# Kernel optimization log

Hardware: AMD Instinct MI355X
Metric: run time of the kernel (lower is better)

Reference implementation:

```python
import jax, jax.numpy as jnp
import numpy as np

H = 16          # num_heads
W = 256         # attention_window
D_MODEL = 1024
D_FF = 4096
EPS = 1e-5


def _layernorm(x, g, b):
    mu = jnp.mean(x, axis=-1, keepdims=True)
    var = jnp.mean(jnp.square(x - mu), axis=-1, keepdims=True)
    return (x - mu) * jax.lax.rsqrt(var + EPS) * g + b


def _sliding_attn(q, k, v, w):
    # q,k,v: [B,H,S,d]; each query attends to keys in [i-w, i+w]
    B, Hh, S, d = q.shape
    nc = S // w
    qc = q.reshape(B, Hh, nc, w, d)
    kp = jnp.pad(k, ((0, 0), (0, 0), (w, w), (0, 0)))
    vp = jnp.pad(v, ((0, 0), (0, 0), (w, w), (0, 0)))
    # gather 3w keys per chunk (prev w, current w, next w)
    idx = (jnp.arange(nc) * w)[:, None] + jnp.arange(3 * w)[None, :]  # [nc, 3w]
    kc = kp[:, :, idx, :]  # [B,H,nc,3w,d]
    vc = vp[:, :, idx, :]
    scores = jnp.einsum('bhcqd,bhckd->bhcqk', qc, kc)  # [B,H,nc,w,3w]
    q_pos = jnp.arange(nc)[:, None, None] * w + jnp.arange(w)[None, :, None]
    k_pos = jnp.arange(nc)[:, None, None] * w - w + jnp.arange(3 * w)[None, None, :]
    rel = k_pos - q_pos
    valid = (jnp.abs(rel) <= w) & (k_pos >= 0) & (k_pos < S)  # [nc,w,3w]
    scores = jnp.where(valid[None, None], scores, jnp.float32(-1e9))
    p = jax.nn.softmax(scores, axis=-1)
    out = jnp.einsum('bhcqk,bhckd->bhcqd', p, vc)
    return out.reshape(B, Hh, S, d)


def setup_inputs() -> dict:
    key = jax.random.key(0)
    ks = jax.random.split(key, 8)
    B, S = 2, 4096
    src = jax.random.normal(ks[0], (B, S, D_MODEL), dtype=jnp.float32)
    ln1_g = jnp.ones((D_MODEL,), jnp.float32)
    ln1_b = jnp.zeros((D_MODEL,), jnp.float32)
    ln2_g = jnp.ones((D_MODEL,), jnp.float32)
    ln2_b = jnp.zeros((D_MODEL,), jnp.float32)
    W1 = jax.random.normal(ks[1], (D_MODEL, D_FF), jnp.float32) * 0.02
    b1 = jnp.zeros((D_FF,), jnp.float32)
    W2 = jax.random.normal(ks[2], (D_FF, D_MODEL), jnp.float32) * 0.02
    b2 = jnp.zeros((D_MODEL,), jnp.float32)
    return {"src": src, "ln1_g": ln1_g, "ln1_b": ln1_b, "ln2_g": ln2_g,
            "ln2_b": ln2_b, "W1": W1, "b1": b1, "W2": W2, "b2": b2}


def reference(src, ln1_g, ln1_b, ln2_g, ln2_b, W1, b1, W2, b2):
    B, S, _ = src.shape
    d_head = D_MODEL // H
    qkv = src.reshape(B, S, H, d_head).transpose(0, 2, 1, 3)  # [B,H,S,d]
    attn = _sliding_attn(qkv, qkv, qkv, W)
    attn = attn.transpose(0, 2, 1, 3).reshape(B, S, D_MODEL)
    x = _layernorm(src + attn, ln1_g, ln1_b)
    ff = jnp.maximum(x @ W1 + b1, 0.0) @ W2 + b2
    return _layernorm(x + ff, ln2_g, ln2_b)
```

## Files before the change

kernel.cpp:

```cpp
#include <hip/hip_runtime.h>

typedef __bf16 bf16x8 __attribute__((ext_vector_type(8)));
typedef __bf16 bf16x4 __attribute__((ext_vector_type(4)));
typedef float f32x4 __attribute__((ext_vector_type(4)));

#define MFMA16(a, b, c) __builtin_amdgcn_mfma_f32_16x16x32_bf16((a), (b), (c), 0, 0, 0)

__device__ __forceinline__ void gload_lds16(const void* g, void* l) {
  __builtin_amdgcn_global_load_lds(
      (const __attribute__((address_space(1))) unsigned int*)g,
      (__attribute__((address_space(3))) unsigned int*)l, 16, 0, 0);
}

__global__ __launch_bounds__(512, 2) void attn_kernel(const float* __restrict__ src,
                                                      float* __restrict__ attn_out) {
  const int bid = blockIdx.x;
  const int c = bid & 15;
  const int h = (bid >> 4) & 15;
  const int b = bid >> 8;
  const int tid = threadIdx.x;
  const int w = tid >> 6;
  const int lane = tid & 63;
  const int lg = lane >> 4;
  const int l16 = lane & 15;
  const size_t b4096 = (size_t)b * 4096;

  __shared__ __bf16 Ks[64][72];
  __shared__ __bf16 Vt[64][72];

  const int q0 = c * 256 + w * 32;
  const float LOG2E = 1.44269504f;

  bf16x8 qf[2][2];
#pragma unroll
  for (int qfi = 0; qfi < 2; ++qfi)
#pragma unroll
    for (int ks = 0; ks < 2; ++ks) {
      const int row = q0 + qfi * 16 + l16;
      const int d0 = ks * 32 + lg * 8;
      const float* p = src + (b4096 + row) * 1024 + h * 64 + d0;
      bf16x8 v;
#pragma unroll
      for (int j = 0; j < 8; ++j) v[j] = (__bf16)(p[j] * LOG2E);
      qf[qfi][ks] = v;
    }

  int krow[4];
#pragma unroll
  for (int kf = 0; kf < 4; ++kf)
    krow[kf] = ((kf >> 1) << 5) + ((l16 >> 2) << 3) + ((kf & 1) << 2) + (l16 & 3);

  const f32x4 z4 = {0.f, 0.f, 0.f, 0.f};
  float m_run[2], l_run[2];
  f32x4 o[2][4];
#pragma unroll
  for (int qfi = 0; qfi < 2; ++qfi) {
    m_run[qfi] = -6.0e8f;
    l_run[qfi] = 0.f;
#pragma unroll
    for (int df = 0; df < 4; ++df) o[qfi][df] = z4;
  }

  const int stage_key = tid >> 3;
  const int stage_d0 = (tid & 7) * 8;
  const int vcol = stage_key ^ stage_d0;

  int kpos = c * 256 - 256 + stage_key;
  float4 ga, gb;
  {
    const int rc = min(max(kpos, 0), 4095);
    const float* p = src + (b4096 + rc) * 1024 + h * 64 + stage_d0;
    ga = *(const float4*)p;
    gb = *(const float4*)(p + 4);
  }

  for (int kt = 0; kt < 12; ++kt) {
    const int kbase = c * 256 - 256 + kt * 64;
    bf16x8 kv;
    const bool inb = ((unsigned)kpos < 4096u);
    kv[0] = (__bf16)(inb ? ga.x : 0.f); kv[1] = (__bf16)(inb ? ga.y : 0.f);
    kv[2] = (__bf16)(inb ? ga.z : 0.f); kv[3] = (__bf16)(inb ? ga.w : 0.f);
    kv[4] = (__bf16)(inb ? gb.x : 0.f); kv[5] = (__bf16)(inb ? gb.y : 0.f);
    kv[6] = (__bf16)(inb ? gb.z : 0.f); kv[7] = (__bf16)(inb ? gb.w : 0.f);

    __syncthreads();
    *(bf16x8*)&Ks[stage_key][stage_d0] = kv;
#pragma unroll
    for (int j = 0; j < 8; ++j) Vt[stage_d0 + j][vcol] = kv[j];
    asm volatile("s_waitcnt lgkmcnt(0)" ::: "memory");
    __builtin_amdgcn_s_barrier();
    __builtin_amdgcn_sched_barrier(0);

    kpos += 64;
    if (kt < 11) {
      const int rc = min(max(kpos, 0), 4095);
      const float* p = src + (b4096 + rc) * 1024 + h * 64 + stage_d0;
      ga = *(const float4*)p;
      gb = *(const float4*)(p + 4);
    }

    const bool skip = (kbase + 63 < 0) | (kbase >= 4096) |
                      (kbase + 63 < q0 - 256) | (kbase > q0 + 31 + 256);
    if (skip) continue;

    f32x4 s[4][2];
#pragma unroll
    for (int kf = 0; kf < 4; ++kf)
#pragma unroll
      for (int qfi = 0; qfi < 2; ++qfi) s[kf][qfi] = z4;

#pragma unroll
    for (int ks = 0; ks < 2; ++ks) {
      bf16x8 ka[4];
#pragma unroll
      for (int kf = 0; kf < 4; ++kf)
        ka[kf] = *(const bf16x8*)&Ks[krow[kf]][ks * 32 + lg * 8];
#pragma unroll
      for (int kf = 0; kf < 4; ++kf)
#pragma unroll
        for (int qfi = 0; qfi < 2; ++qfi)
          s[kf][qfi] = MFMA16(ka[kf], qf[qfi][ks], s[kf][qfi]);
    }

    const bool needmask = (kbase < 0) | (kbase > 4032) |
                          (kbase < q0 - 225) | (kbase > q0 + 193);
    if (needmask) {
#pragma unroll
      for (int qfi = 0; qfi < 2; ++qfi) {
        const int qp = q0 + qfi * 16 + l16;
#pragma unroll
        for (int kf = 0; kf < 4; ++kf) {
          const int kb0 = kbase + ((kf >> 1) << 5) + 8 * lg + ((kf & 1) << 2);
#pragma unroll
          for (int reg = 0; reg < 4; ++reg) {
            const int kp = kb0 + reg;
            const int rel = kp - qp;
            if (rel > 256 || rel < -256 || kp < 0 || kp >= 4096)
              s[kf][qfi][reg] = -1e9f;
          }
        }
      }
    }

    bf16x4 pb[4][2];
#pragma unroll
    for (int qfi = 0; qfi < 2; ++qfi) {
      float tm = s[0][qfi][0];
#pragma unroll
      for (int kf = 0; kf < 4; ++kf)
#pragma unroll
        for (int reg = 0; reg < 4; ++reg) tm = fmaxf(tm, s[kf][qfi][reg]);
      tm = fmaxf(tm, __shfl_xor(tm, 16, 64));
      tm = fmaxf(tm, __shfl_xor(tm, 32, 64));

      const float mn = fmaxf(m_run[qfi], tm);
      const float scl = exp2f(m_run[qfi] - mn);
      m_run[qfi] = mn;

      float rs = 0.f;
#pragma unroll
      for (int kf = 0; kf < 4; ++kf) {
        bf16x4 pv;
#pragma unroll
        for (int reg = 0; reg < 4; ++reg) {
          const float p = exp2f(s[kf][qfi][reg] - mn);
          rs += p;
          pv[reg] = (__bf16)p;
        }
        pb[kf][qfi] = pv;
      }
      rs += __shfl_xor(rs, 16, 64);
      rs += __shfl_xor(rs, 32, 64);
      l_run[qfi] = l_run[qfi] * scl + rs;

#pragma unroll
      for (int df = 0; df < 4; ++df)
#pragma unroll
        for (int reg = 0; reg < 4; ++reg) o[qfi][df][reg] *= scl;
    }

#pragma unroll
    for (int ks2 = 0; ks2 < 2; ++ks2) {
      bf16x8 av[4];
#pragma unroll
      for (int df = 0; df < 4; ++df) {
        const int d = df * 16 + l16;
        const int blk = (ks2 * 4 + lg) ^ (d >> 3);
        av[df] = *(const bf16x8*)&Vt[d][blk * 8];
      }
#pragma unroll
      for (int qfi = 0; qfi < 2; ++qfi) {
        const bf16x8 bq = __builtin_shufflevector(pb[2 * ks2][qfi], pb[2 * ks2 + 1][qfi],
                                                  0, 1, 2, 3, 4, 5, 6, 7);
#pragma unroll
        for (int df = 0; df < 4; ++df)
          o[qfi][df] = MFMA16(av[df], bq, o[qfi][df]);
      }
    }
  }

#pragma unroll
  for (int qfi = 0; qfi < 2; ++qfi) {
    const float inv = 1.0f / l_run[qfi];
    const int qp = q0 + qfi * 16 + l16;
    float* dst = attn_out + (b4096 + qp) * 1024 + h * 64 + lg * 4;
#pragma unroll
    for (int df = 0; df < 4; ++df) {
      float4 r;
      r.x = o[qfi][df][0] * inv;
      r.y = o[qfi][df][1] * inv;
      r.z = o[qfi][df][2] * inv;
      r.w = o[qfi][df][3] * inv;
      *(float4*)&dst[df * 16] = r;
    }
  }
}

template <int MODE>
__global__ __launch_bounds__(512, 2) void gemm8p(const __bf16* __restrict__ A,
                                                 const __bf16* __restrict__ Bt,
                                                 const float* __restrict__ bias,
                                                 void* __restrict__ out0,
                                                 void* __restrict__ out1,
                                                 int M, int N, int Kstride, int Klen) {
  __shared__ char smem[131072];
  const int tid = threadIdx.x;
  const int w = tid >> 6;
  const int lane = tid & 63;
  const int lg = lane >> 4;
  const int l16 = lane & 15;
  const int wr = w >> 2;
  const int wc = w & 3;

  const int nbn = N >> 8;
  const int x = ((int)blockIdx.x & 7) * ((int)gridDim.x >> 3) + ((int)blockIdx.x >> 3);
  const long bm = (long)(x / nbn) * 256;
  const long bn = (long)(x % nbn) * 256;
  const long koff = (long)blockIdx.y * Klen;
  void* out = blockIdx.y ? out1 : out0;

  const f32x4 z4 = {0.f, 0.f, 0.f, 0.f};
  f32x4 acc[8][4];
#pragma unroll
  for (int i = 0; i < 8; ++i)
#pragma unroll
    for (int j = 0; j < 4; ++j) acc[i][j] = z4;

  const int srow = tid >> 2;
  const int g0 = (tid & 3) ^ ((tid >> 3) & 3);
  const __bf16* Ag = A + (size_t)(bm + srow) * Kstride + koff + g0 * 8;
  const __bf16* Bg = Bt + (size_t)(bn + srow) * Kstride + koff + g0 * 8;

  auto stage = [&](int kt, int osel, int isB, int khalf) {
    const __bf16* src = (isB ? Bg : Ag) + (size_t)kt * 64 + khalf * 32;
    char* dst = smem + (isB ? 65536 : 0) + osel * 32768 + khalf * 16384 + (w << 10);
    gload_lds16(src, dst);
    gload_lds16(src + (size_t)128 * Kstride, dst + 8192);
  };

  const int lslot = (lg ^ ((l16 >> 1) & 3)) << 4;
  const char* pA = smem + (wr * 128 + l16) * 64 + lslot;
  const char* pB = smem + 65536 + (wc * 64 + l16) * 64 + lslot;
  auto rdA = [&](int sel, int rf, int ks) {
    return *(const bf16x8*)(pA + sel * 32768 + ks * 16384 + rf * 1024);
  };
  auto rdB = [&](int sel, int cf, int ks) {
    return *(const bf16x8*)(pB + sel * 32768 + ks * 16384 + cf * 1024);
  };

  const int NT = Klen >> 6;

  stage(0, 0, 0, 0);
  stage(0, 0, 1, 0);
  stage(0, 0, 0, 1);
  stage(0, 0, 1, 1);
  asm volatile("s_waitcnt vmcnt(4)" ::: "memory");
  __builtin_amdgcn_s_barrier();
  __builtin_amdgcn_sched_barrier(0);

  for (int t = 0; t < NT; ++t) {
    const int sel = t & 1, osel = sel ^ 1;
    const bool st = (t + 1) < NT;
    bf16x8 af[8], bf[4];

#pragma unroll
    for (int rf = 0; rf < 8; ++rf) af[rf] = rdA(sel, rf, 0);
#pragma unroll
    for (int cf = 0; cf < 4; ++cf) bf[cf] = rdB(sel, cf, 0);
    if (st) { stage(t + 1, osel, 0, 0); stage(t + 1, osel, 1, 0); }
    __builtin_amdgcn_s_setprio(1);
#pragma unroll
    for (int rf = 0; rf < 8; ++rf)
#pragma unroll
      for (int cf = 0; cf < 4; ++cf)
        acc[rf][cf] = MFMA16(af[rf], bf[cf], acc[rf][cf]);
    __builtin_amdgcn_s_setprio(0);
    if (st) asm volatile("s_waitcnt vmcnt(4)" ::: "memory");
    else    asm volatile("s_waitcnt vmcnt(0)" ::: "memory");
    __builtin_amdgcn_s_barrier();
    __builtin_amdgcn_sched_barrier(0);

#pragma unroll
    for (int rf = 0; rf < 8; ++rf) af[rf] = rdA(sel, rf, 1);
#pragma unroll
    for (int cf = 0; cf < 4; ++cf) bf[cf] = rdB(sel, cf, 1);
    if (st) { stage(t + 1, osel, 0, 1); stage(t + 1, osel, 1, 1); }
    __builtin_amdgcn_s_setprio(1);
#pragma unroll
    for (int rf = 0; rf < 8; ++rf)
#pragma unroll
      for (int cf = 0; cf < 4; ++cf)
        acc[rf][cf] = MFMA16(af[rf], bf[cf], acc[rf][cf]);
    __builtin_amdgcn_s_setprio(0);
    if (st) asm volatile("s_waitcnt vmcnt(4)" ::: "memory");
    __builtin_amdgcn_s_barrier();
    __builtin_amdgcn_sched_barrier(0);
  }

  float bv[4];
  if (MODE == 0) {
#pragma unroll
    for (int cf = 0; cf < 4; ++cf) bv[cf] = bias[bn + wc * 64 + cf * 16 + l16];
  }
#pragma unroll
  for (int rf = 0; rf < 8; ++rf)
#pragma unroll
    for (int reg = 0; reg < 4; ++reg) {
      const long row = bm + wr * 128 + rf * 16 + lg * 4 + reg;
#pragma unroll
      for (int cf = 0; cf < 4; ++cf) {
        const long col = bn + wc * 64 + cf * 16 + l16;
        if (MODE == 0) {
          const float v = fmaxf(acc[rf][cf][reg] + bv[cf], 0.f);
          ((__bf16*)out)[row * N + col] = (__bf16)v;
        } else {
          ((float*)out)[row * N + col] = acc[rf][cf][reg];
        }
      }
    }
}

__global__ __launch_bounds__(256) void transpose_cvt(const float* __restrict__ in,
                                                     __bf16* __restrict__ out,
                                                     int R, int C) {
  __shared__ float tile[64][65];
  const long r0 = (long)blockIdx.y * 64;
  const long c0 = (long)blockIdx.x * 64;
  const int t = threadIdx.x;
  const int tr = t >> 6;
  const int tc = t & 63;
#pragma unroll
  for (int i = 0; i < 16; ++i) {
    const int r = tr * 16 + i;
    tile[r][tc] = in[(r0 + r) * C + c0 + tc];
  }
  __syncthreads();
#pragma unroll
  for (int i = 0; i < 16; ++i) {
    const int cc = tr * 16 + i;
    out[(c0 + cc) * (long)R + r0 + tc] = (__bf16)tile[tc][cc];
  }
}

__global__ __launch_bounds__(256) void ln1_kernel(const float* __restrict__ src,
                                                  const float* __restrict__ attn,
                                                  const float* __restrict__ g,
                                                  const float* __restrict__ bta,
                                                  __bf16* __restrict__ xb) {
  const long r = blockIdx.x;
  const int t = threadIdx.x;
  const float4 a = *(const float4*)&src[r * 1024 + t * 4];
  const float4 cc = *(const float4*)&attn[r * 1024 + t * 4];
  float v[4] = {a.x + cc.x, a.y + cc.y, a.z + cc.z, a.w + cc.w};
  float s = v[0] + v[1] + v[2] + v[3];
  float s2 = v[0] * v[0] + v[1] * v[1] + v[2] * v[2] + v[3] * v[3];
#pragma unroll
  for (int off = 32; off >= 1; off >>= 1) {
    s += __shfl_xor(s, off, 64);
    s2 += __shfl_xor(s2, off, 64);
  }
  __shared__ float red[8];
  if ((t & 63) == 0) { red[t >> 6] = s; red[(t >> 6) + 4] = s2; }
  __syncthreads();
  s = red[0] + red[1] + red[2] + red[3];
  s2 = red[4] + red[5] + red[6] + red[7];
  const float mu = s * (1.f / 1024.f);
  const float var = s2 * (1.f / 1024.f) - mu * mu;
  const float rstd = rsqrtf(var + 1e-5f);
  const float4 gv = *(const float4*)&g[t * 4];
  const float4 bv = *(const float4*)&bta[t * 4];
  bf16x4 y;
  y[0] = (__bf16)((v[0] - mu) * rstd * gv.x + bv.x);
  y[1] = (__bf16)((v[1] - mu) * rstd * gv.y + bv.y);
  y[2] = (__bf16)((v[2] - mu) * rstd * gv.z + bv.z);
  y[3] = (__bf16)((v[3] - mu) * rstd * gv.w + bv.w);
  *(bf16x4*)&xb[r * 1024 + t * 4] = y;
}

__global__ __launch_bounds__(256) void ln2_kernel(const __bf16* __restrict__ xb,
                                                  const float* __restrict__ f0,
                                                  const float* __restrict__ f1,
                                                  const float* __restrict__ b2,
                                                  const float* __restrict__ g,
                                                  const float* __restrict__ bta,
                                                  float* __restrict__ out) {
  const long r = blockIdx.x;
  const int t = threadIdx.x;
  const bf16x4 xv = *(const bf16x4*)&xb[r * 1024 + t * 4];
  const float4 f0v = *(const float4*)&f0[r * 1024 + t * 4];
  const float4 f1v = *(const float4*)&f1[r * 1024 + t * 4];
  const float4 b2v = *(const float4*)&b2[t * 4];
  float v[4] = {(float)xv[0] + f0v.x + f1v.x + b2v.x,
                (float)xv[1] + f0v.y + f1v.y + b2v.y,
                (float)xv[2] + f0v.z + f1v.z + b2v.z,
                (float)xv[3] + f0v.w + f1v.w + b2v.w};
  float s = v[0] + v[1] + v[2] + v[3];
  float s2 = v[0] * v[0] + v[1] * v[1] + v[2] * v[2] + v[3] * v[3];
#pragma unroll
  for (int off = 32; off >= 1; off >>= 1) {
    s += __shfl_xor(s, off, 64);
    s2 += __shfl_xor(s2, off, 64);
  }
  __shared__ float red[8];
  if ((t & 63) == 0) { red[t >> 6] = s; red[(t >> 6) + 4] = s2; }
  __syncthreads();
  s = red[0] + red[1] + red[2] + red[3];
  s2 = red[4] + red[5] + red[6] + red[7];
  const float mu = s * (1.f / 1024.f);
  const float var = s2 * (1.f / 1024.f) - mu * mu;
  const float rstd = rsqrtf(var + 1e-5f);
  const float4 gv = *(const float4*)&g[t * 4];
  const float4 bv = *(const float4*)&bta[t * 4];
  float4 y;
  y.x = (v[0] - mu) * rstd * gv.x + bv.x;
  y.y = (v[1] - mu) * rstd * gv.y + bv.y;
  y.z = (v[2] - mu) * rstd * gv.z + bv.z;
  y.w = (v[3] - mu) * rstd * gv.w + bv.w;
  *(float4*)&out[r * 1024 + t * 4] = y;
}

extern "C" void kernel_launch(void* const* d_in, const int* in_sizes, int n_in,
                              void* d_out, int out_size, void* d_ws, size_t ws_size,
                              hipStream_t stream) {
  const float* src = (const float*)d_in[0];
  const float* ln1_g = (const float*)d_in[1];
  const float* ln1_b = (const float*)d_in[2];
  const float* ln2_g = (const float*)d_in[3];
  const float* ln2_b = (const float*)d_in[4];
  const float* W1 = (const float*)d_in[5];
  const float* b1 = (const float*)d_in[6];
  const float* W2 = (const float*)d_in[7];
  const float* b2 = (const float*)d_in[8];
  float* out = (float*)d_out;
  char* ws = (char*)d_ws;

  const size_t MB = 1048576;
  float* ff0 = (float*)ws;
  float* ff1 = (float*)(ws + 32 * MB);
  __bf16* xb = (__bf16*)(ws + 64 * MB);
  __bf16* w1t = (__bf16*)(ws + 80 * MB);
  __bf16* w2t = (__bf16*)(ws + 88 * MB);
  __bf16* hbuf = (__bf16*)(ws + 96 * MB);

  int Mc = 8192;
  while (Mc > 512 && 96 * MB + (size_t)Mc * 8192 > ws_size) Mc >>= 1;

  transpose_cvt<<<dim3(4096 / 64, 1024 / 64), 256, 0, stream>>>(W1, w1t, 1024, 4096);
  transpose_cvt<<<dim3(1024 / 64, 4096 / 64), 256, 0, stream>>>(W2, w2t, 4096, 1024);
  attn_kernel<<<512, 512, 0, stream>>>(src, ff0);
  ln1_kernel<<<8192, 256, 0, stream>>>(src, ff0, ln1_g, ln1_b, xb);
  for (int m0 = 0; m0 < 8192; m0 += Mc) {
    gemm8p<0><<<dim3((Mc / 256) * (4096 / 256), 1), 512, 0, stream>>>(
        xb + (size_t)m0 * 1024, w1t, b1, hbuf, hbuf, Mc, 4096, 1024, 1024);
    gemm8p<1><<<dim3((Mc / 256) * (1024 / 256), 2), 512, 0, stream>>>(
        hbuf, w2t, nullptr, ff0 + (size_t)m0 * 1024, ff1 + (size_t)m0 * 1024,
        Mc, 1024, 4096, 2048);
  }
  ln2_kernel<<<8192, 256, 0, stream>>>(xb, ff0, ff1, b2, ln2_g, ln2_b, out);
}
```

Before: 253.3 us.

## Deepen GEMM LDS pipeline, double-buffer attention K/V, skip softmax rescales

The GEMM main loop moves from a two-buffer, 64-wide k-step scheme with two barriers per step to a four-slot ring of 32-wide k-steps. Loads are issued three steps ahead, with one barrier per step and graded vmcnt waits, so more global-to-LDS latency is hidden. The attention kernel double-buffers its K and V tiles in LDS, which removes the leading __syncthreads per key tile. Its online softmax skips the running-max update and output rescale unless some lane's tile max exceeds the running max by more than 8 in log2 space. That trades fewer multiplies for larger bf16 probabilities and some precision risk.

After: 248.7 us. About the same (-1.8%).

```diff
diff --git a/kernel.cpp b/kernel.cpp
--- a/kernel.cpp
+++ b/kernel.cpp
@@ -25,8 +25,8 @@
   const int l16 = lane & 15;
   const size_t b4096 = (size_t)b * 4096;
 
-  __shared__ __bf16 Ks[64][72];
-  __shared__ __bf16 Vt[64][72];
+  __shared__ __bf16 Ks[2][64][72];
+  __shared__ __bf16 Vt[2][64][72];
 
   const int q0 = c * 256 + w * 32;
   const float LOG2E = 1.44269504f;
@@ -76,6 +76,7 @@
 
   for (int kt = 0; kt < 12; ++kt) {
     const int kbase = c * 256 - 256 + kt * 64;
+    const int cur = kt & 1;
     bf16x8 kv;
     const bool inb = ((unsigned)kpos < 4096u);
     kv[0] = (__bf16)(inb ? ga.x : 0.f); kv[1] = (__bf16)(inb ? ga.y : 0.f);
@@ -83,10 +84,9 @@
     kv[4] = (__bf16)(inb ? gb.x : 0.f); kv[5] = (__bf16)(inb ? gb.y : 0.f);
     kv[6] = (__bf16)(inb ? gb.z : 0.f); kv[7] = (__bf16)(inb ? gb.w : 0.f);
 
-    __syncthreads();
-    *(bf16x8*)&Ks[stage_key][stage_d0] = kv;
-#pragma unroll
-    for (int j = 0; j < 8; ++j) Vt[stage_d0 + j][vcol] = kv[j];
+    *(bf16x8*)&Ks[cur][stage_key][stage_d0] = kv;
+#pragma unroll
+    for (int j = 0; j < 8; ++j) Vt[cur][stage_d0 + j][vcol] = kv[j];
     asm volatile("s_waitcnt lgkmcnt(0)" ::: "memory");
     __builtin_amdgcn_s_barrier();
     __builtin_amdgcn_sched_barrier(0);
@@ -114,7 +114,7 @@
       bf16x8 ka[4];
 #pragma unroll
       for (int kf = 0; kf < 4; ++kf)
-        ka[kf] = *(const bf16x8*)&Ks[krow[kf]][ks * 32 + lg * 8];
+        ka[kf] = *(const bf16x8*)&Ks[cur][krow[kf]][ks * 32 + lg * 8];
 #pragma unroll
       for (int kf = 0; kf < 4; ++kf)
 #pragma unroll
@@ -153,9 +153,18 @@
       tm = fmaxf(tm, __shfl_xor(tm, 16, 64));
       tm = fmaxf(tm, __shfl_xor(tm, 32, 64));
 
-      const float mn = fmaxf(m_run[qfi], tm);
-      const float scl = exp2f(m_run[qfi] - mn);
-      m_run[qfi] = mn;
+      const bool nomax = __all(tm <= m_run[qfi] + 8.f);
+      float scl = 1.f;
+      if (!nomax) {
+        const float mn = fmaxf(m_run[qfi], tm);
+        scl = exp2f(m_run[qfi] - mn);
+        m_run[qfi] = mn;
+#pragma unroll
+        for (int df = 0; df < 4; ++df)
+#pragma unroll
+          for (int reg = 0; reg < 4; ++reg) o[qfi][df][reg] *= scl;
+      }
+      const float mn = m_run[qfi];
 
       float rs = 0.f;
 #pragma unroll
@@ -172,11 +181,6 @@
       rs += __shfl_xor(rs, 16, 64);
       rs += __shfl_xor(rs, 32, 64);
       l_run[qfi] = l_run[qfi] * scl + rs;
-
-#pragma unroll
-      for (int df = 0; df < 4; ++df)
-#pragma unroll
-        for (int reg = 0; reg < 4; ++reg) o[qfi][df][reg] *= scl;
     }
 
 #pragma unroll
@@ -186,7 +190,7 @@
       for (int df = 0; df < 4; ++df) {
         const int d = df * 16 + l16;
         const int blk = (ks2 * 4 + lg) ^ (d >> 3);
-        av[df] = *(const bf16x8*)&Vt[d][blk * 8];
+        av[df] = *(const bf16x8*)&Vt[cur][d][blk * 8];
       }
 #pragma unroll
       for (int qfi = 0; qfi < 2; ++qfi) {
@@ -251,43 +255,42 @@
   const __bf16* Ag = A + (size_t)(bm + srow) * Kstride + koff + g0 * 8;
   const __bf16* Bg = Bt + (size_t)(bn + srow) * Kstride + koff + g0 * 8;
 
-  auto stage = [&](int kt, int osel, int isB, int khalf) {
-    const __bf16* src = (isB ? Bg : Ag) + (size_t)kt * 64 + khalf * 32;
-    char* dst = smem + (isB ? 65536 : 0) + osel * 32768 + khalf * 16384 + (w << 10);
-    gload_lds16(src, dst);
-    gload_lds16(src + (size_t)128 * Kstride, dst + 8192);
+  auto stage = [&](int kt) {
+    char* da = smem + ((kt & 3) << 15) + (w << 10);
+    const size_t o = (size_t)kt * 32;
+    gload_lds16(Ag + o, da);
+    gload_lds16(Ag + o + (size_t)128 * Kstride, da + 8192);
+    gload_lds16(Bg + o, da + 16384);
+    gload_lds16(Bg + o + (size_t)128 * Kstride, da + 16384 + 8192);
   };
 
   const int lslot = (lg ^ ((l16 >> 1) & 3)) << 4;
   const char* pA = smem + (wr * 128 + l16) * 64 + lslot;
-  const char* pB = smem + 65536 + (wc * 64 + l16) * 64 + lslot;
-  auto rdA = [&](int sel, int rf, int ks) {
-    return *(const bf16x8*)(pA + sel * 32768 + ks * 16384 + rf * 1024);
+  const char* pB = smem + 16384 + (wc * 64 + l16) * 64 + lslot;
+  auto rdA = [&](int buf, int rf) {
+    return *(const bf16x8*)(pA + (buf << 15) + rf * 1024);
   };
-  auto rdB = [&](int sel, int cf, int ks) {
-    return *(const bf16x8*)(pB + sel * 32768 + ks * 16384 + cf * 1024);
+  auto rdB = [&](int buf, int cf) {
+    return *(const bf16x8*)(pB + (buf << 15) + cf * 1024);
   };
 
-  const int NT = Klen >> 6;
-
-  stage(0, 0, 0, 0);
-  stage(0, 0, 1, 0);
-  stage(0, 0, 0, 1);
-  stage(0, 0, 1, 1);
-  asm volatile("s_waitcnt vmcnt(4)" ::: "memory");
+  const int NT = Klen >> 5;
+
+  stage(0); stage(1); stage(2); stage(3);
+  asm volatile("s_waitcnt vmcnt(12)" ::: "memory");
   __builtin_amdgcn_s_barrier();
   __builtin_amdgcn_sched_barrier(0);
 
   for (int t = 0; t < NT; ++t) {
-    const int sel = t & 1, osel = sel ^ 1;
-    const bool st = (t + 1) < NT;
+    const int buf = t & 3;
+    if (t > 0 && t + 3 < NT) stage(t + 3);
+
     bf16x8 af[8], bf[4];
-
-#pragma unroll
-    for (int rf = 0; rf < 8; ++rf) af[rf] = rdA(sel, rf, 0);
-#pragma unroll
-    for (int cf = 0; cf < 4; ++cf) bf[cf] = rdB(sel, cf, 0);
-    if (st) { stage(t + 1, osel, 0, 0); stage(t + 1, osel, 1, 0); }
+#pragma unroll
+    for (int rf = 0; rf < 8; ++rf) af[rf] = rdA(buf, rf);
+#pragma unroll
+    for (int cf = 0; cf < 4; ++cf) bf[cf] = rdB(buf, cf);
+
     __builtin_amdgcn_s_setprio(1);
 #pragma unroll
     for (int rf = 0; rf < 8; ++rf)
@@ -295,24 +298,11 @@
       for (int cf = 0; cf < 4; ++cf)
         acc[rf][cf] = MFMA16(af[rf], bf[cf], acc[rf][cf]);
     __builtin_amdgcn_s_setprio(0);
-    if (st) asm volatile("s_waitcnt vmcnt(4)" ::: "memory");
-    else    asm volatile("s_waitcnt vmcnt(0)" ::: "memory");
-    __builtin_amdgcn_s_barrier();
-    __builtin_amdgcn_sched_barrier(0);
-
-#pragma unroll
-    for (int rf = 0; rf < 8; ++rf) af[rf] = rdA(sel, rf, 1);
-#pragma unroll
-    for (int cf = 0; cf < 4; ++cf) bf[cf] = rdB(sel, cf, 1);
-    if (st) { stage(t + 1, osel, 0, 1); stage(t + 1, osel, 1, 1); }
-    __builtin_amdgcn_s_setprio(1);
-#pragma unroll
-    for (int rf = 0; rf < 8; ++rf)
-#pragma unroll
-      for (int cf = 0; cf < 4; ++cf)
-        acc[rf][cf] = MFMA16(af[rf], bf[cf], acc[rf][cf]);
-    __builtin_amdgcn_s_setprio(0);
-    if (st) asm volatile("s_waitcnt vmcnt(4)" ::: "memory");
+
+    const int nfly = min(2, NT - 2 - t);
+    if (nfly >= 2)      asm volatile("s_waitcnt vmcnt(8)" ::: "memory");
+    else if (nfly == 1) asm volatile("s_waitcnt vmcnt(4)" ::: "memory");
+    else                asm volatile("s_waitcnt vmcnt(0)" ::: "memory");
     __builtin_amdgcn_s_barrier();
     __builtin_amdgcn_sched_barrier(0);
   }
```
